# Performance work log

Measured on AMD Instinct MI355X. Metric: run time of the kernel, lower is better.

Reference implementation:

```python
import jax, jax.numpy as jnp
import numpy as np
import math

NEIGHBOR_RADIUS = 30.0

def _masked_softmax(logits, mask, axis):
    # mask: bool, True = keep; all-masked rows return zeros
    p = jax.nn.softmax(jnp.where(mask, logits, -1e9), axis=axis) * mask.astype(logits.dtype)
    return p / jnp.clip(jnp.sum(p, axis=axis, keepdims=True), 1e-9, None)

def _forward(agents_state, agents_mask, map_polylines, map_poly_mask,
             map_poly_type, map_tl_status, map_on_route,
             pm_w1, pm_b1, pm_w2, pm_b2, type_emb, tl_emb, route_emb,
             mo_w1, mo_b1, mo_w2, mo_b2,
             ae_w1, ae_b1, ae_w2, ae_b2, ae_w3, ae_b3,
             mr_w1, mr_b1, mr_w2, mr_b2,
             nr_w1, nr_b1, nr_w2, nr_b2,
             to_w1, to_b1, to_w2, to_b2):
    relu = jax.nn.relu
    a_mask = (agents_mask > 0.5).astype(agents_state.dtype)   # (B,N,T)
    a_feat = agents_state[..., :5]
    # ---- map polyline node encoder ----
    h = relu(map_polylines @ pm_w1 + pm_b1)                   # (B,M,L,H)
    h = relu(h @ pm_w2 + pm_b2)
    h = h.max(axis=2)                                         # (B,M,H) max-pool over points
    t_idx = jnp.clip(map_poly_type, 0, type_emb.shape[0] - 1)
    s_idx = jnp.clip(map_tl_status, 0, tl_emb.shape[0] - 1)
    r_idx = jnp.clip(map_on_route, 0, route_emb.shape[0] - 1)
    h = h + type_emb[t_idx] + tl_emb[s_idx] + route_emb[r_idx]
    h = relu(h @ mo_w1 + mo_b1) @ mo_w2 + mo_b2
    map_mask = map_poly_mask > 0.5                            # (B,M) bool
    map_node = h * map_mask[..., None].astype(h.dtype)        # (B,M,D)
    map_center = map_polylines.mean(axis=2)                   # (B,M,2)
    # ---- agent state encoder ----
    a = relu(a_feat @ ae_w1 + ae_b1)
    a = relu(a @ ae_w2 + ae_b2)
    a_emb = (a @ ae_w3 + ae_b3) * a_mask[..., None]           # (B,N,T,D)
    D = a_emb.shape[-1]
    # ---- agent -> map attention ----
    agent_pos = a_feat[..., 0:2]
    rel = map_center[:, None, None, :, :] - agent_pos[:, :, :, None, :]  # (B,N,T,M,2)
    dist = jnp.linalg.norm(rel, axis=-1, keepdims=True)
    rel_feat = jnp.concatenate([rel, dist], axis=-1)          # (B,N,T,M,3)
    rel_score = (relu(rel_feat @ mr_w1 + mr_b1) @ mr_w2 + mr_b2)[..., 0]  # (B,N,T,M)
    dot = jnp.einsum('bntd,bmd->bntm', a_emb, map_node) / math.sqrt(D)
    score_mask = jnp.broadcast_to(map_mask[:, None, None, :], dot.shape)
    attn = _masked_softmax(dot + rel_score, score_mask, axis=-1)
    map_ctx = jnp.einsum('bntm,bmd->bntd', attn, map_node)    # (B,N,T,D)
    # ---- neighbor graph attention ----
    pos = a_feat[..., 0:2]
    vel = a_feat[..., 3:5]
    pos_j = jnp.transpose(pos, (0, 2, 1, 3))                  # (B,T,N,2)
    vel_j = jnp.transpose(vel, (0, 2, 1, 3))
    rel_pos = pos_j[:, None, :, :, :] - pos[:, :, :, None, :] # (B,N,T,N,2) = p_j - p_i
    rel_vel = vel_j[:, None, :, :, :] - vel[:, :, :, None, :]
    dist_ij = jnp.linalg.norm(rel_pos, axis=-1, keepdims=True)
    rel_ij = jnp.concatenate([rel_pos, rel_vel, dist_ij], axis=-1)        # (B,N,T,N,5)
    nbr_score = (relu(rel_ij @ nr_w1 + nr_b1) @ nr_w2 + nr_b2)[..., 0]    # (B,N,T,N)
    am_b = agents_mask > 0.5
    valid_i = am_b[..., None]                                 # (B,N,T,1)
    valid_j = jnp.transpose(am_b, (0, 2, 1))[:, None, :, :]   # (B,1,T,N)
    N = pos.shape[1]
    not_self = ~jnp.eye(N, dtype=bool)[None, :, None, :]      # (1,N,1,N)
    nbr_mask = valid_i & valid_j & (dist_ij[..., 0] <= NEIGHBOR_RADIUS) & not_self
    dot_n = jnp.einsum('bitd,bjtd->bitj', a_emb, a_emb) / math.sqrt(D)
    w_n = _masked_softmax(dot_n + nbr_score, nbr_mask, axis=-1)
    nbr_ctx = jnp.einsum('bitj,bjtd->bitd', w_n, a_emb)       # (B,N,T,D)
    # ---- tau head ----
    tau = jnp.concatenate([a_emb, map_ctx, nbr_ctx], axis=-1)
    tau = relu(tau @ to_w1 + to_b1) @ to_w2 + to_b2
    return tau * a_mask[..., None]

def setup_inputs() -> dict:
    key = jax.random.key(0)
    B, N, T, M, L = 2, 32, 32, 256, 20
    H, D, TAU = 128, 128, 64
    ks = jax.random.split(key, 32)
    def f(i, shp):
        return jax.random.normal(ks[i], shp, jnp.float32) * 0.05
    inp = {}
    inp['agents_state'] = jax.random.normal(ks[0], (B, N, T, 5), jnp.float32) * jnp.array([50., 50., 1., 5., 5.], jnp.float32)
    inp['agents_mask'] = jnp.ones((B, N, T), jnp.float32)
    inp['map_polylines'] = jax.random.normal(ks[1], (B, M, L, 2), jnp.float32) * 50.0
    inp['map_poly_mask'] = jnp.ones((B, M), jnp.float32)
    inp['map_poly_type'] = jax.random.randint(ks[2], (B, M), 0, 4)
    inp['map_tl_status'] = jax.random.randint(ks[3], (B, M), 0, 8)
    inp['map_on_route'] = jax.random.randint(ks[4], (B, M), 0, 2)
    inp['pm_w1'] = f(5, (2, H));  inp['pm_b1'] = jnp.zeros((H,), jnp.float32)
    inp['pm_w2'] = f(6, (H, H)); inp['pm_b2'] = jnp.zeros((H,), jnp.float32)
    inp['type_emb'] = f(7, (4, H)); inp['tl_emb'] = f(8, (8, H)); inp['route_emb'] = f(9, (2, H))
    inp['mo_w1'] = f(10, (H, H)); inp['mo_b1'] = jnp.zeros((H,), jnp.float32)
    inp['mo_w2'] = f(11, (H, D)); inp['mo_b2'] = jnp.zeros((D,), jnp.float32)
    inp['ae_w1'] = f(12, (5, H)); inp['ae_b1'] = jnp.zeros((H,), jnp.float32)
    inp['ae_w2'] = f(13, (H, H)); inp['ae_b2'] = jnp.zeros((H,), jnp.float32)
    inp['ae_w3'] = f(14, (H, D)); inp['ae_b3'] = jnp.zeros((D,), jnp.float32)
    inp['mr_w1'] = f(15, (3, H)); inp['mr_b1'] = jnp.zeros((H,), jnp.float32)
    inp['mr_w2'] = f(16, (H, 1)); inp['mr_b2'] = jnp.zeros((1,), jnp.float32)
    inp['nr_w1'] = f(17, (5, H)); inp['nr_b1'] = jnp.zeros((H,), jnp.float32)
    inp['nr_w2'] = f(18, (H, 1)); inp['nr_b2'] = jnp.zeros((1,), jnp.float32)
    inp['to_w1'] = f(19, (3 * D, H)); inp['to_b1'] = jnp.zeros((H,), jnp.float32)
    inp['to_w2'] = f(20, (H, TAU)); inp['to_b2'] = jnp.zeros((TAU,), jnp.float32)
    return inp

def reference(agents_state, agents_mask, map_polylines, map_poly_mask,
              map_poly_type, map_tl_status, map_on_route,
              pm_w1, pm_b1, pm_w2, pm_b2, type_emb, tl_emb, route_emb,
              mo_w1, mo_b1, mo_w2, mo_b2,
              ae_w1, ae_b1, ae_w2, ae_b2, ae_w3, ae_b3,
              mr_w1, mr_b1, mr_w2, mr_b2,
              nr_w1, nr_b1, nr_w2, nr_b2,
              to_w1, to_b1, to_w2, to_b2):
    return _forward(agents_state, agents_mask, map_polylines, map_poly_mask,
                    map_poly_type, map_tl_status, map_on_route,
                    pm_w1, pm_b1, pm_w2, pm_b2, type_emb, tl_emb, route_emb,
                    mo_w1, mo_b1, mo_w2, mo_b2,
                    ae_w1, ae_b1, ae_w2, ae_b2, ae_w3, ae_b3,
                    mr_w1, mr_b1, mr_w2, mr_b2,
                    nr_w1, nr_b1, nr_w2, nr_b2,
                    to_w1, to_b1, to_w2, to_b2)
```

## Files before the change

### kernel.cpp

```cpp
#include <hip/hip_runtime.h>

#define RSQRT_D 0.08838834764831843f

__global__ __launch_bounds__(256) void kAB_front(
    const float* __restrict__ poly, const float* __restrict__ pmask,
    const int* __restrict__ ptype, const int* __restrict__ ptl, const int* __restrict__ proute,
    const float* __restrict__ pm_w1, const float* __restrict__ pm_b1,
    const float* __restrict__ pm_w2, const float* __restrict__ pm_b2,
    const float* __restrict__ type_emb, const float* __restrict__ tl_emb, const float* __restrict__ route_emb,
    const float* __restrict__ mo_w1, const float* __restrict__ mo_b1,
    const float* __restrict__ mo_w2, const float* __restrict__ mo_b2,
    const float* __restrict__ astate, const float* __restrict__ amask,
    const float* __restrict__ ae_w1, const float* __restrict__ ae_b1,
    const float* __restrict__ ae_w2, const float* __restrict__ ae_b2,
    const float* __restrict__ ae_w3, const float* __restrict__ ae_b3,
    float* __restrict__ map_node, float* __restrict__ map_nodeT, float* __restrict__ center,
    float* __restrict__ a_emb, float* __restrict__ aT, float* __restrict__ posT)
{
    int tid = threadIdx.x;
    if (blockIdx.x < 512) {
        int bm = blockIdx.x;
        int b = bm >> 8, m = bm & 255;
        int h = tid & 127, rw = tid >> 7;
        __shared__ float xch[2][128];
        __shared__ __align__(16) float hvs[128];
        __shared__ __align__(16) float g2[128];

        const float* pp = poly + bm*40 + rw*20;
        float xs[10], ys[10];
        #pragma unroll
        for (int u = 0; u < 10; ++u) { xs[u] = pp[2*u]; ys[u] = pp[2*u+1]; }
        float acc[10];
        #pragma unroll
        for (int u = 0; u < 10; ++u) acc[u] = 0.f;
        #pragma unroll 4
        for (int k = 0; k < 128; ++k) {
            float w2v = pm_w2[k*128 + h];
            float wx = pm_w1[k], wy = pm_w1[128+k], bb = pm_b1[k];
            #pragma unroll
            for (int u = 0; u < 10; ++u) {
                float h1 = fmaxf(fmaf(wx, xs[u], fmaf(wy, ys[u], bb)), 0.f);
                acc[u] = fmaf(h1, w2v, acc[u]);
            }
        }
        float mx = acc[0];
        #pragma unroll
        for (int u = 1; u < 10; ++u) mx = fmaxf(mx, acc[u]);
        xch[rw][h] = mx;
        __syncthreads();
        if (rw == 0) {
            float v = fmaxf(fmaxf(mx, xch[1][h]) + pm_b2[h], 0.f);
            int ti = min(max(ptype[bm],0),3);
            int si = min(max(ptl[bm],0),7);
            int ri = min(max(proute[bm],0),1);
            hvs[h] = v + type_emb[ti*128+h] + tl_emb[si*128+h] + route_emb[ri*128+h];
        }
        __syncthreads();
        if (rw == 0) {
            float a1 = mo_b1[h];
            for (int kc = 0; kc < 32; ++kc) {
                float4 xv = *(const float4*)&hvs[kc*4];
                a1 = fmaf(xv.x, mo_w1[(kc*4+0)*128+h],
                     fmaf(xv.y, mo_w1[(kc*4+1)*128+h],
                     fmaf(xv.z, mo_w1[(kc*4+2)*128+h],
                     fmaf(xv.w, mo_w1[(kc*4+3)*128+h], a1))));
            }
            g2[h] = fmaxf(a1, 0.f);
        }
        __syncthreads();
        if (rw == 0) {
            float a2 = mo_b2[h];
            for (int kc = 0; kc < 32; ++kc) {
                float4 xv = *(const float4*)&g2[kc*4];
                a2 = fmaf(xv.x, mo_w2[(kc*4+0)*128+h],
                     fmaf(xv.y, mo_w2[(kc*4+1)*128+h],
                     fmaf(xv.z, mo_w2[(kc*4+2)*128+h],
                     fmaf(xv.w, mo_w2[(kc*4+3)*128+h], a2))));
            }
            float mk = (pmask[bm] > 0.5f) ? 1.f : 0.f;
            a2 *= mk;
            map_node[bm*128 + h] = a2;
            map_nodeT[(b*128+h)*256 + m] = a2;
        }
        if (tid == 0) {
            float sx = 0.f, sy = 0.f;
            #pragma unroll
            for (int l = 0; l < 20; ++l) { sx += poly[bm*40 + 2*l]; sy += poly[bm*40 + 2*l + 1]; }
            center[bm*2+0] = sx * 0.05f;
            center[bm*2+1] = sy * 0.05f;
        }
    } else {
        int h = tid & 127, rp = tid >> 7;
        int r0 = (blockIdx.x - 512)*8 + rp*4;
        __shared__ float f5[2][4][5];
        __shared__ __align__(16) float a1s[2][4][128];
        if (h < 20) f5[rp][h/5][h%5] = astate[(r0 + h/5)*5 + (h%5)];
        __syncthreads();
        float b1v = ae_b1[h];
        float v[4];
        {
            float w0 = ae_w1[h], w1 = ae_w1[128+h], w2 = ae_w1[256+h], w3 = ae_w1[384+h], w4 = ae_w1[512+h];
            #pragma unroll
            for (int r = 0; r < 4; ++r) {
                float a = b1v;
                a = fmaf(f5[rp][r][0], w0, a); a = fmaf(f5[rp][r][1], w1, a);
                a = fmaf(f5[rp][r][2], w2, a); a = fmaf(f5[rp][r][3], w3, a);
                a = fmaf(f5[rp][r][4], w4, a);
                v[r] = fmaxf(a, 0.f);
            }
        }
        #pragma unroll
        for (int r = 0; r < 4; ++r) a1s[rp][r][h] = v[r];
        __syncthreads();
        {
            float b2v = ae_b2[h];
            float a0 = b2v, a1 = b2v, a2 = b2v, a3 = b2v;
            for (int kc = 0; kc < 32; ++kc) {
                float4 x0 = *(const float4*)&a1s[rp][0][kc*4];
                float4 x1 = *(const float4*)&a1s[rp][1][kc*4];
                float4 x2 = *(const float4*)&a1s[rp][2][kc*4];
                float4 x3 = *(const float4*)&a1s[rp][3][kc*4];
                float w0 = ae_w2[(kc*4+0)*128+h], w1 = ae_w2[(kc*4+1)*128+h];
                float w2 = ae_w2[(kc*4+2)*128+h], w3 = ae_w2[(kc*4+3)*128+h];
                a0 = fmaf(x0.x,w0,fmaf(x0.y,w1,fmaf(x0.z,w2,fmaf(x0.w,w3,a0))));
                a1 = fmaf(x1.x,w0,fmaf(x1.y,w1,fmaf(x1.z,w2,fmaf(x1.w,w3,a1))));
                a2 = fmaf(x2.x,w0,fmaf(x2.y,w1,fmaf(x2.z,w2,fmaf(x2.w,w3,a2))));
                a3 = fmaf(x3.x,w0,fmaf(x3.y,w1,fmaf(x3.z,w2,fmaf(x3.w,w3,a3))));
            }
            v[0]=fmaxf(a0,0.f); v[1]=fmaxf(a1,0.f); v[2]=fmaxf(a2,0.f); v[3]=fmaxf(a3,0.f);
        }
        __syncthreads();
        #pragma unroll
        for (int r = 0; r < 4; ++r) a1s[rp][r][h] = v[r];
        __syncthreads();
        {
            float b3v = ae_b3[h];
            float a0 = b3v, a1 = b3v, a2 = b3v, a3 = b3v;
            for (int kc = 0; kc < 32; ++kc) {
                float4 x0 = *(const float4*)&a1s[rp][0][kc*4];
                float4 x1 = *(const float4*)&a1s[rp][1][kc*4];
                float4 x2 = *(const float4*)&a1s[rp][2][kc*4];
                float4 x3 = *(const float4*)&a1s[rp][3][kc*4];
                float w0 = ae_w3[(kc*4+0)*128+h], w1 = ae_w3[(kc*4+1)*128+h];
                float w2 = ae_w3[(kc*4+2)*128+h], w3 = ae_w3[(kc*4+3)*128+h];
                a0 = fmaf(x0.x,w0,fmaf(x0.y,w1,fmaf(x0.z,w2,fmaf(x0.w,w3,a0))));
                a1 = fmaf(x1.x,w0,fmaf(x1.y,w1,fmaf(x1.z,w2,fmaf(x1.w,w3,a1))));
                a2 = fmaf(x2.x,w0,fmaf(x2.y,w1,fmaf(x2.z,w2,fmaf(x2.w,w3,a2))));
                a3 = fmaf(x3.x,w0,fmaf(x3.y,w1,fmaf(x3.z,w2,fmaf(x3.w,w3,a3))));
            }
            v[0]=a0; v[1]=a1; v[2]=a2; v[3]=a3;
        }
        #pragma unroll
        for (int r = 0; r < 4; ++r) {
            int rr = r0 + r;
            float mk = (amask[rr] > 0.5f) ? 1.f : 0.f;
            float e = v[r] * mk;
            a_emb[rr*128 + h] = e;
            int bb = rr >> 10, nn = (rr >> 5) & 31, tt = rr & 31;
            int bt = bb*32 + tt;
            aT[(bt*128 + h)*32 + nn] = e;
        }
        if (h < 20) {
            int r = h / 5, c = h % 5;
            int rr = r0 + r;
            int bb = rr >> 10, nn = (rr >> 5) & 31, tt = rr & 31;
            int bt = bb*32 + tt;
            float val;
            if      (c == 0) val = f5[rp][r][0];
            else if (c == 1) val = f5[rp][r][1];
            else if (c == 2) val = f5[rp][r][3];
            else if (c == 3) val = f5[rp][r][4];
            else             val = amask[rr];
            posT[(bt*5 + c)*32 + nn] = val;
        }
    }
}

__global__ __launch_bounds__(256) void kC_attn(
    const float* __restrict__ astate, const float* __restrict__ amask,
    const float* __restrict__ pmask,
    const float* __restrict__ a_emb, const float* __restrict__ map_node,
    const float* __restrict__ map_nodeT, const float* __restrict__ center,
    const float* __restrict__ mr_w1, const float* __restrict__ mr_b1,
    const float* __restrict__ mr_w2, const float* __restrict__ mr_b2,
    const float* __restrict__ aT, const float* __restrict__ posT,
    const float* __restrict__ nr_w1, const float* __restrict__ nr_b1,
    const float* __restrict__ nr_w2, const float* __restrict__ nr_b2,
    float* __restrict__ map_ctx, float* __restrict__ p_n)
{
    int tid = threadIdx.x;
    int lam = tid & 63, wv = tid >> 6;
    __shared__ float lg4[4][256];
    __shared__ __align__(16) float p4[256*4];
    __shared__ float ctxp[4][128];

    if (blockIdx.x < 512) {
        int r0 = blockIdx.x * 4;
        int b = r0 >> 10;
        int m = tid;
        float rx[4], ry[4], dd[4], dt[4], sA[4];
        float b2c = mr_b2[0];
        float cx = center[(b*256+m)*2+0], cy = center[(b*256+m)*2+1];
        #pragma unroll
        for (int r = 0; r < 4; ++r) {
            float px = astate[(r0+r)*5+0], py = astate[(r0+r)*5+1];
            rx[r] = cx - px; ry[r] = cy - py;
            dd[r] = sqrtf(rx[r]*rx[r] + ry[r]*ry[r]);
            dt[r] = 0.f; sA[r] = b2c;
        }
        #pragma unroll 8
        for (int hh = 0; hh < 128; ++hh) {
            float wa = mr_w1[hh], wb = mr_w1[128+hh], wc = mr_w1[256+hh];
            float bb = mr_b1[hh], w2 = mr_w2[hh];
            #pragma unroll
            for (int r = 0; r < 4; ++r) {
                float t1 = fmaf(rx[r], wa, fmaf(ry[r], wb, fmaf(dd[r], wc, bb)));
                sA[r] = fmaf(fmaxf(t1, 0.f), w2, sA[r]);
            }
        }
        const float* mT = map_nodeT + b*128*256 + m;
        #pragma unroll 8
        for (int d = 0; d < 128; ++d) {
            float v = mT[d*256];
            #pragma unroll
            for (int r = 0; r < 4; ++r)
                dt[r] = fmaf(v, a_emb[(r0+r)*128 + d], dt[r]);
        }
        bool mk = pmask[b*256+m] > 0.5f;
        #pragma unroll
        for (int r = 0; r < 4; ++r)
            lg4[r][m] = mk ? fmaf(dt[r], RSQRT_D, sA[r]) : -1e30f;
        __syncthreads();
        {
            float x0 = lg4[wv][lam], x1 = lg4[wv][64+lam], x2 = lg4[wv][128+lam], x3 = lg4[wv][192+lam];
            float mxv = fmaxf(fmaxf(x0,x1), fmaxf(x2,x3));
            #pragma unroll
            for (int off = 32; off; off >>= 1) mxv = fmaxf(mxv, __shfl_xor(mxv, off));
            float e0 = (x0 > -1e29f) ? expf(x0-mxv) : 0.f;
            float e1 = (x1 > -1e29f) ? expf(x1-mxv) : 0.f;
            float e2 = (x2 > -1e29f) ? expf(x2-mxv) : 0.f;
            float e3 = (x3 > -1e29f) ? expf(x3-mxv) : 0.f;
            float sm = e0+e1+e2+e3;
            #pragma unroll
            for (int off = 32; off; off >>= 1) sm += __shfl_xor(sm, off);
            float inv = 1.f / fmaxf(sm, 1e-9f);
            p4[lam*4 + wv]       = e0*inv;
            p4[(64+lam)*4 + wv]  = e1*inv;
            p4[(128+lam)*4 + wv] = e2*inv;
            p4[(192+lam)*4 + wv] = e3*inv;
        }
        __syncthreads();
        {
            int d = tid & 127, hf = tid >> 7;
            float ac0 = 0.f, ac1 = 0.f, ac2 = 0.f, ac3 = 0.f;
            const float* mn = map_node + (b*256 + hf*128)*128 + d;
            const float4* pp = (const float4*)p4 + hf*128;
            #pragma unroll 4
            for (int mm = 0; mm < 128; ++mm) {
                float4 pv = pp[mm];
                float v = mn[mm*128];
                ac0 = fmaf(pv.x, v, ac0); ac1 = fmaf(pv.y, v, ac1);
                ac2 = fmaf(pv.z, v, ac2); ac3 = fmaf(pv.w, v, ac3);
            }
            if (hf == 1) { ctxp[0][d]=ac0; ctxp[1][d]=ac1; ctxp[2][d]=ac2; ctxp[3][d]=ac3; }
            __syncthreads();
            if (hf == 0) {
                map_ctx[(r0+0)*128+d] = ac0 + ctxp[0][d];
                map_ctx[(r0+1)*128+d] = ac1 + ctxp[1][d];
                map_ctx[(r0+2)*128+d] = ac2 + ctxp[2][d];
                map_ctx[(r0+3)*128+d] = ac3 + ctxp[3][d];
            }
        }
    } else {
        int r = (blockIdx.x - 512)*4 + wv;
        int b = r >> 10, ii = (r >> 5) & 31, tt = r & 31;
        int bt = b*32 + tt;
        int j = lam & 31, hs = lam >> 5;
        float pxi = astate[r*5+0], pyi = astate[r*5+1], vxi = astate[r*5+3], vyi = astate[r*5+4];
        const float* pT = posT + bt*160;
        float pxj = pT[j], pyj = pT[32+j], vxj = pT[64+j], vyj = pT[96+j], mj = pT[128+j];
        float rpx = pxj-pxi, rpy = pyj-pyi, rvx = vxj-vxi, rvy = vyj-vyi;
        float ddv = sqrtf(rpx*rpx + rpy*rpy);
        const float* ei = a_emb + (size_t)r*128;
        const float* aTp = aT + (size_t)bt*4096 + j;
        float s = 0.f, dot = 0.f;
        int h0 = hs*64;
        #pragma unroll 8
        for (int q = 0; q < 64; ++q) {
            int hh = h0 + q;
            float wA = nr_w1[hh], wB = nr_w1[128+hh], wC = nr_w1[256+hh];
            float wD = nr_w1[384+hh], wE = nr_w1[512+hh];
            float bb = nr_b1[hh], w2 = nr_w2[hh];
            float t1 = fmaf(rpx, wA, fmaf(rpy, wB, fmaf(rvx, wC,
                       fmaf(rvy, wD, fmaf(ddv, wE, bb)))));
            s = fmaf(fmaxf(t1, 0.f), w2, s);
            dot = fmaf(ei[hh], aTp[hh*32], dot);
        }
        s   += __shfl_xor(s, 32);
        dot += __shfl_xor(dot, 32);
        bool vi = amask[r] > 0.5f, vj = mj > 0.5f;
        bool ok = vi && vj && (ddv <= 30.0f) && (j != ii);
        float lg = ok ? fmaf(dot, RSQRT_D, s + nr_b2[0]) : -1e30f;
        float mxv = lg;
        #pragma unroll
        for (int off = 16; off; off >>= 1) mxv = fmaxf(mxv, __shfl_xor(mxv, off));
        float e = (lg > -1e29f) ? expf(lg - mxv) : 0.f;
        float sm = e;
        #pragma unroll
        for (int off = 16; off; off >>= 1) sm += __shfl_xor(sm, off);
        if (hs == 0) p_n[r*32 + j] = e / fmaxf(sm, 1e-9f);
    }
}

__global__ __launch_bounds__(256) void kD_out(
    const float* __restrict__ amask, const float* __restrict__ a_emb,
    const float* __restrict__ map_ctx, const float* __restrict__ p_n,
    const float* __restrict__ to_w1, const float* __restrict__ to_b1,
    const float* __restrict__ to_w2, const float* __restrict__ to_b2,
    float* __restrict__ out)
{
    int r0 = blockIdx.x * 4;
    int b = r0 >> 10, t0 = r0 & 31;
    int tid = threadIdx.x;
    __shared__ __align__(16) float tau[4][384];
    __shared__ float redn[4][128];
    __shared__ __align__(16) float gpart[4][4][128];
    __shared__ __align__(16) float g1s[4][128];

    for (int q = tid; q < 512; q += 256) {
        int rr = q >> 7, d = q & 127;
        tau[rr][d]       = a_emb[(r0+rr)*128 + d];
        tau[rr][128 + d] = map_ctx[(r0+rr)*128 + d];
    }
    __syncthreads();
    {
        int d = tid & 127, hf = tid >> 7;
        float ac[4] = {0.f,0.f,0.f,0.f};
        for (int jj = 0; jj < 16; ++jj) {
            int j2 = hf*16 + jj;
            float p0 = p_n[(r0+0)*32 + j2];
            float p1 = p_n[(r0+1)*32 + j2];
            float p2 = p_n[(r0+2)*32 + j2];
            float p3 = p_n[(r0+3)*32 + j2];
            const float* ejb = a_emb + (size_t)((b*32 + j2)*32 + t0)*128 + d;
            ac[0] = fmaf(p0, ejb[0],   ac[0]);
            ac[1] = fmaf(p1, ejb[128], ac[1]);
            ac[2] = fmaf(p2, ejb[256], ac[2]);
            ac[3] = fmaf(p3, ejb[384], ac[3]);
        }
        if (hf == 1) { redn[0][d]=ac[0]; redn[1][d]=ac[1]; redn[2][d]=ac[2]; redn[3][d]=ac[3]; }
        __syncthreads();
        if (hf == 0) {
            #pragma unroll
            for (int r = 0; r < 4; ++r) tau[r][256 + d] = ac[r] + redn[r][d];
        }
    }
    __syncthreads();
    {
        int h6 = tid & 63, kq = tid >> 6;
        float aL[4] = {0.f,0.f,0.f,0.f};
        float aH[4] = {0.f,0.f,0.f,0.f};
        for (int c = 0; c < 24; ++c) {
            int k4 = kq*24 + c;
            float4 x0 = *(const float4*)&tau[0][k4*4];
            float4 x1 = *(const float4*)&tau[1][k4*4];
            float4 x2 = *(const float4*)&tau[2][k4*4];
            float4 x3 = *(const float4*)&tau[3][k4*4];
            float wl0 = to_w1[(k4*4+0)*128 + h6], wh0 = to_w1[(k4*4+0)*128 + 64+h6];
            float wl1 = to_w1[(k4*4+1)*128 + h6], wh1 = to_w1[(k4*4+1)*128 + 64+h6];
            float wl2 = to_w1[(k4*4+2)*128 + h6], wh2 = to_w1[(k4*4+2)*128 + 64+h6];
            float wl3 = to_w1[(k4*4+3)*128 + h6], wh3 = to_w1[(k4*4+3)*128 + 64+h6];
            aL[0]=fmaf(x0.x,wl0,fmaf(x0.y,wl1,fmaf(x0.z,wl2,fmaf(x0.w,wl3,aL[0]))));
            aH[0]=fmaf(x0.x,wh0,fmaf(x0.y,wh1,fmaf(x0.z,wh2,fmaf(x0.w,wh3,aH[0]))));
            aL[1]=fmaf(x1.x,wl0,fmaf(x1.y,wl1,fmaf(x1.z,wl2,fmaf(x1.w,wl3,aL[1]))));
            aH[1]=fmaf(x1.x,wh0,fmaf(x1.y,wh1,fmaf(x1.z,wh2,fmaf(x1.w,wh3,aH[1]))));
            aL[2]=fmaf(x2.x,wl0,fmaf(x2.y,wl1,fmaf(x2.z,wl2,fmaf(x2.w,wl3,aL[2]))));
            aH[2]=fmaf(x2.x,wh0,fmaf(x2.y,wh1,fmaf(x2.z,wh2,fmaf(x2.w,wh3,aH[2]))));
            aL[3]=fmaf(x3.x,wl0,fmaf(x3.y,wl1,fmaf(x3.z,wl2,fmaf(x3.w,wl3,aL[3]))));
            aH[3]=fmaf(x3.x,wh0,fmaf(x3.y,wh1,fmaf(x3.z,wh2,fmaf(x3.w,wh3,aH[3]))));
        }
        #pragma unroll
        for (int r = 0; r < 4; ++r) {
            gpart[kq][r][h6]      = aL[r];
            gpart[kq][r][64 + h6] = aH[r];
        }
    }
    __syncthreads();
    {
        int h = tid & 127, rp = tid >> 7;
        float bv = to_b1[h];
        #pragma unroll
        for (int rr = rp; rr < 4; rr += 2) {
            float s = gpart[0][rr][h] + gpart[1][rr][h] + gpart[2][rr][h] + gpart[3][rr][h];
            g1s[rr][h] = fmaxf(s + bv, 0.f);
        }
    }
    __syncthreads();
    {
        int o = tid & 63, row = tid >> 6;
        float a2 = to_b2[o];
        for (int kc = 0; kc < 32; ++kc) {
            float4 g = *(const float4*)&g1s[row][kc*4];
            a2 = fmaf(g.x, to_w2[(kc*4+0)*64 + o],
                 fmaf(g.y, to_w2[(kc*4+1)*64 + o],
                 fmaf(g.z, to_w2[(kc*4+2)*64 + o],
                 fmaf(g.w, to_w2[(kc*4+3)*64 + o], a2))));
        }
        float mk = (amask[r0+row] > 0.5f) ? 1.f : 0.f;
        out[(r0+row)*64 + o] = a2 * mk;
    }
}

extern "C" void kernel_launch(void* const* d_in, const int* in_sizes, int n_in,
                              void* d_out, int out_size, void* d_ws, size_t ws_size,
                              hipStream_t stream) {
    const float* agents_state  = (const float*)d_in[0];
    const float* agents_mask   = (const float*)d_in[1];
    const float* map_polylines = (const float*)d_in[2];
    const float* map_poly_mask = (const float*)d_in[3];
    const int*   map_poly_type = (const int*)d_in[4];
    const int*   map_tl_status = (const int*)d_in[5];
    const int*   map_on_route  = (const int*)d_in[6];
    const float* pm_w1 = (const float*)d_in[7];
    const float* pm_b1 = (const float*)d_in[8];
    const float* pm_w2 = (const float*)d_in[9];
    const float* pm_b2 = (const float*)d_in[10];
    const float* type_emb  = (const float*)d_in[11];
    const float* tl_emb    = (const float*)d_in[12];
    const float* route_emb = (const float*)d_in[13];
    const float* mo_w1 = (const float*)d_in[14];
    const float* mo_b1 = (const float*)d_in[15];
    const float* mo_w2 = (const float*)d_in[16];
    const float* mo_b2 = (const float*)d_in[17];
    const float* ae_w1 = (const float*)d_in[18];
    const float* ae_b1 = (const float*)d_in[19];
    const float* ae_w2 = (const float*)d_in[20];
    const float* ae_b2 = (const float*)d_in[21];
    const float* ae_w3 = (const float*)d_in[22];
    const float* ae_b3 = (const float*)d_in[23];
    const float* mr_w1 = (const float*)d_in[24];
    const float* mr_b1 = (const float*)d_in[25];
    const float* mr_w2 = (const float*)d_in[26];
    const float* mr_b2 = (const float*)d_in[27];
    const float* nr_w1 = (const float*)d_in[28];
    const float* nr_b1 = (const float*)d_in[29];
    const float* nr_w2 = (const float*)d_in[30];
    const float* nr_b2 = (const float*)d_in[31];
    const float* to_w1 = (const float*)d_in[32];
    const float* to_b1 = (const float*)d_in[33];
    const float* to_w2 = (const float*)d_in[34];
    const float* to_b2 = (const float*)d_in[35];

    float* ws = (float*)d_ws;
    float* map_node  = ws;
    float* map_nodeT = ws + 65536;
    float* center    = ws + 131072;
    float* a_emb     = ws + 132096;
    float* aT        = ws + 394240;
    float* posT      = ws + 656384;
    float* map_ctx   = ws + 666624;
    float* p_n       = ws + 928768;

    float* out = (float*)d_out;

    kAB_front<<<768, 256, 0, stream>>>(map_polylines, map_poly_mask,
        map_poly_type, map_tl_status, map_on_route,
        pm_w1, pm_b1, pm_w2, pm_b2, type_emb, tl_emb, route_emb,
        mo_w1, mo_b1, mo_w2, mo_b2,
        agents_state, agents_mask,
        ae_w1, ae_b1, ae_w2, ae_b2, ae_w3, ae_b3,
        map_node, map_nodeT, center, a_emb, aT, posT);

    kC_attn<<<1024, 256, 0, stream>>>(agents_state, agents_mask, map_poly_mask,
        a_emb, map_node, map_nodeT, center,
        mr_w1, mr_b1, mr_w2, mr_b2,
        aT, posT,
        nr_w1, nr_b1, nr_w2, nr_b2,
        map_ctx, p_n);

    kD_out<<<512, 256, 0, stream>>>(agents_mask, a_emb, map_ctx, p_n,
        to_w1, to_b1, to_w2, to_b2, out);
}
```

Baseline: 188.9 us.

## Fuse attention and output kernels; stage polyline hidden layer in shared memory

The map-attention, neighbor-attention and output-MLP kernels are merged into one 512-thread kernel per 4-row group. The map and neighbor halves run in parallel thread groups, and context vectors and neighbor probabilities pass through shared memory instead of global buffers. This removes one launch and the map_ctx/p_n round trip to global memory. Separately, the polyline encoder now computes the first-layer activations once per hidden unit into shared memory rather than recomputing them inside the k loop. The cost is larger blocks and more shared memory, which can lower occupancy, and half the threads sit idle in the later stages.

```diff
diff --git a/kernel.cpp b/kernel.cpp
--- a/kernel.cpp
+++ b/kernel.cpp
@@ -25,23 +25,48 @@
         __shared__ float xch[2][128];
         __shared__ __align__(16) float hvs[128];
         __shared__ __align__(16) float g2[128];
-
-        const float* pp = poly + bm*40 + rw*20;
-        float xs[10], ys[10];
-        #pragma unroll
-        for (int u = 0; u < 10; ++u) { xs[u] = pp[2*u]; ys[u] = pp[2*u+1]; }
-        float acc[10];
-        #pragma unroll
-        for (int u = 0; u < 10; ++u) acc[u] = 0.f;
-        #pragma unroll 4
-        for (int k = 0; k < 128; ++k) {
-            float w2v = pm_w2[k*128 + h];
+        __shared__ __align__(16) float h1s[2][128][12];
+
+        {
+            int k = h;
+            int half = rw;
+            const float* pp = poly + bm*40 + half*20;
             float wx = pm_w1[k], wy = pm_w1[128+k], bb = pm_b1[k];
+            float h1v[10];
             #pragma unroll
             for (int u = 0; u < 10; ++u) {
-                float h1 = fmaxf(fmaf(wx, xs[u], fmaf(wy, ys[u], bb)), 0.f);
-                acc[u] = fmaf(h1, w2v, acc[u]);
-            }
+                float x = pp[2*u], y = pp[2*u+1];
+                h1v[u] = fmaxf(fmaf(wx, x, fmaf(wy, y, bb)), 0.f);
+            }
+            float4 s0 = make_float4(h1v[0], h1v[1], h1v[2], h1v[3]);
+            float4 s1 = make_float4(h1v[4], h1v[5], h1v[6], h1v[7]);
+            float2 s2 = make_float2(h1v[8], h1v[9]);
+            *(float4*)&h1s[half][k][0] = s0;
+            *(float4*)&h1s[half][k][4] = s1;
+            *(float2*)&h1s[half][k][8] = s2;
+        }
+        __syncthreads();
+
+        float acc[10];
+        #pragma unroll
+        for (int u = 0; u < 10; ++u) acc[u] = 0.f;
+        const float* w2p = pm_w2 + h;
+        #pragma unroll 2
+        for (int k = 0; k < 128; ++k) {
+            float w2v = w2p[k*128];
+            float4 A  = *(const float4*)&h1s[rw][k][0];
+            float4 Bv = *(const float4*)&h1s[rw][k][4];
+            float2 Cv = *(const float2*)&h1s[rw][k][8];
+            acc[0] = fmaf(A.x,  w2v, acc[0]);
+            acc[1] = fmaf(A.y,  w2v, acc[1]);
+            acc[2] = fmaf(A.z,  w2v, acc[2]);
+            acc[3] = fmaf(A.w,  w2v, acc[3]);
+            acc[4] = fmaf(Bv.x, w2v, acc[4]);
+            acc[5] = fmaf(Bv.y, w2v, acc[5]);
+            acc[6] = fmaf(Bv.z, w2v, acc[6]);
+            acc[7] = fmaf(Bv.w, w2v, acc[7]);
+            acc[8] = fmaf(Cv.x, w2v, acc[8]);
+            acc[9] = fmaf(Cv.y, w2v, acc[9]);
         }
         float mx = acc[0];
         #pragma unroll
@@ -176,7 +201,7 @@
     }
 }
 
-__global__ __launch_bounds__(256) void kC_attn(
+__global__ __launch_bounds__(512) void kCD_fused(
     const float* __restrict__ astate, const float* __restrict__ amask,
     const float* __restrict__ pmask,
     const float* __restrict__ a_emb, const float* __restrict__ map_node,
@@ -186,17 +211,24 @@
     const float* __restrict__ aT, const float* __restrict__ posT,
     const float* __restrict__ nr_w1, const float* __restrict__ nr_b1,
     const float* __restrict__ nr_w2, const float* __restrict__ nr_b2,
-    float* __restrict__ map_ctx, float* __restrict__ p_n)
+    const float* __restrict__ to_w1, const float* __restrict__ to_b1,
+    const float* __restrict__ to_w2, const float* __restrict__ to_b2,
+    float* __restrict__ out)
 {
     int tid = threadIdx.x;
-    int lam = tid & 63, wv = tid >> 6;
+    int r0 = blockIdx.x * 4;
+    int b = r0 >> 10, t0 = r0 & 31;
+
     __shared__ float lg4[4][256];
     __shared__ __align__(16) float p4[256*4];
     __shared__ float ctxp[4][128];
-
-    if (blockIdx.x < 512) {
-        int r0 = blockIdx.x * 4;
-        int b = r0 >> 10;
+    __shared__ float pj[4][32];
+    __shared__ __align__(16) float tau[4][384];
+    __shared__ float redn[4][128];
+    __shared__ __align__(16) float gpart[4][4][128];
+    __shared__ __align__(16) float g1s[4][128];
+
+    if (tid < 256) {
         int m = tid;
         float rx[4], ry[4], dd[4], dt[4], sA[4];
         float b2c = mr_b2[0];
@@ -230,50 +262,10 @@
         #pragma unroll
         for (int r = 0; r < 4; ++r)
             lg4[r][m] = mk ? fmaf(dt[r], RSQRT_D, sA[r]) : -1e30f;
-        __syncthreads();
-        {
-            float x0 = lg4[wv][lam], x1 = lg4[wv][64+lam], x2 = lg4[wv][128+lam], x3 = lg4[wv][192+lam];
-            float mxv = fmaxf(fmaxf(x0,x1), fmaxf(x2,x3));
-            #pragma unroll
-            for (int off = 32; off; off >>= 1) mxv = fmaxf(mxv, __shfl_xor(mxv, off));
-            float e0 = (x0 > -1e29f) ? expf(x0-mxv) : 0.f;
-            float e1 = (x1 > -1e29f) ? expf(x1-mxv) : 0.f;
-            float e2 = (x2 > -1e29f) ? expf(x2-mxv) : 0.f;
-            float e3 = (x3 > -1e29f) ? expf(x3-mxv) : 0.f;
-            float sm = e0+e1+e2+e3;
-            #pragma unroll
-            for (int off = 32; off; off >>= 1) sm += __shfl_xor(sm, off);
-            float inv = 1.f / fmaxf(sm, 1e-9f);
-            p4[lam*4 + wv]       = e0*inv;
-            p4[(64+lam)*4 + wv]  = e1*inv;
-            p4[(128+lam)*4 + wv] = e2*inv;
-            p4[(192+lam)*4 + wv] = e3*inv;
-        }
-        __syncthreads();
-        {
-            int d = tid & 127, hf = tid >> 7;
-            float ac0 = 0.f, ac1 = 0.f, ac2 = 0.f, ac3 = 0.f;
-            const float* mn = map_node + (b*256 + hf*128)*128 + d;
-            const float4* pp = (const float4*)p4 + hf*128;
-            #pragma unroll 4
-            for (int mm = 0; mm < 128; ++mm) {
-                float4 pv = pp[mm];
-                float v = mn[mm*128];
-                ac0 = fmaf(pv.x, v, ac0); ac1 = fmaf(pv.y, v, ac1);
-                ac2 = fmaf(pv.z, v, ac2); ac3 = fmaf(pv.w, v, ac3);
-            }
-            if (hf == 1) { ctxp[0][d]=ac0; ctxp[1][d]=ac1; ctxp[2][d]=ac2; ctxp[3][d]=ac3; }
-            __syncthreads();
-            if (hf == 0) {
-                map_ctx[(r0+0)*128+d] = ac0 + ctxp[0][d];
-                map_ctx[(r0+1)*128+d] = ac1 + ctxp[1][d];
-                map_ctx[(r0+2)*128+d] = ac2 + ctxp[2][d];
-                map_ctx[(r0+3)*128+d] = ac3 + ctxp[3][d];
-            }
-        }
     } else {
-        int r = (blockIdx.x - 512)*4 + wv;
-        int b = r >> 10, ii = (r >> 5) & 31, tt = r & 31;
+        int lam = tid & 63, wv = (tid >> 6) & 3;
+        int r = r0 + wv;
+        int ii = (r >> 5) & 31, tt = r & 31;
         int bt = b*32 + tt;
         int j = lam & 31, hs = lam >> 5;
         float pxi = astate[r*5+0], pyi = astate[r*5+1], vxi = astate[r*5+3], vyi = astate[r*5+4];
@@ -308,55 +300,85 @@
         float sm = e;
         #pragma unroll
         for (int off = 16; off; off >>= 1) sm += __shfl_xor(sm, off);
-        if (hs == 0) p_n[r*32 + j] = e / fmaxf(sm, 1e-9f);
-    }
-}
-
-__global__ __launch_bounds__(256) void kD_out(
-    const float* __restrict__ amask, const float* __restrict__ a_emb,
-    const float* __restrict__ map_ctx, const float* __restrict__ p_n,
-    const float* __restrict__ to_w1, const float* __restrict__ to_b1,
-    const float* __restrict__ to_w2, const float* __restrict__ to_b2,
-    float* __restrict__ out)
-{
-    int r0 = blockIdx.x * 4;
-    int b = r0 >> 10, t0 = r0 & 31;
-    int tid = threadIdx.x;
-    __shared__ __align__(16) float tau[4][384];
-    __shared__ float redn[4][128];
-    __shared__ __align__(16) float gpart[4][4][128];
-    __shared__ __align__(16) float g1s[4][128];
-
-    for (int q = tid; q < 512; q += 256) {
-        int rr = q >> 7, d = q & 127;
-        tau[rr][d]       = a_emb[(r0+rr)*128 + d];
-        tau[rr][128 + d] = map_ctx[(r0+rr)*128 + d];
-    }
-    __syncthreads();
-    {
+        if (hs == 0) pj[wv][j] = e / fmaxf(sm, 1e-9f);
+    }
+    __syncthreads();
+
+    if (tid < 256) {
+        int lam = tid & 63, wv = tid >> 6;
+        float x0 = lg4[wv][lam], x1 = lg4[wv][64+lam], x2 = lg4[wv][128+lam], x3 = lg4[wv][192+lam];
+        float mxv = fmaxf(fmaxf(x0,x1), fmaxf(x2,x3));
+        #pragma unroll
+        for (int off = 32; off; off >>= 1) mxv = fmaxf(mxv, __shfl_xor(mxv, off));
+        float e0 = (x0 > -1e29f) ? expf(x0-mxv) : 0.f;
+        float e1 = (x1 > -1e29f) ? expf(x1-mxv) : 0.f;
+        float e2 = (x2 > -1e29f) ? expf(x2-mxv) : 0.f;
+        float e3 = (x3 > -1e29f) ? expf(x3-mxv) : 0.f;
+        float sm = e0+e1+e2+e3;
+        #pragma unroll
+        for (int off = 32; off; off >>= 1) sm += __shfl_xor(sm, off);
+        float inv = 1.f / fmaxf(sm, 1e-9f);
+        p4[lam*4 + wv]       = e0*inv;
+        p4[(64+lam)*4 + wv]  = e1*inv;
+        p4[(128+lam)*4 + wv] = e2*inv;
+        p4[(192+lam)*4 + wv] = e3*inv;
+    } else {
+        int idx = tid - 256;
+        int d = idx & 127, rr = idx >> 7;
+        tau[rr][d]   = a_emb[(r0+rr)*128 + d];
+        tau[rr+2][d] = a_emb[(r0+rr+2)*128 + d];
+    }
+    __syncthreads();
+
+    float pv0 = 0.f, pv1 = 0.f, pv2 = 0.f, pv3 = 0.f;
+    if (tid < 256) {
         int d = tid & 127, hf = tid >> 7;
-        float ac[4] = {0.f,0.f,0.f,0.f};
+        const float* mn = map_node + (b*256 + hf*128)*128 + d;
+        const float4* ppv = (const float4*)p4 + hf*128;
+        #pragma unroll 4
+        for (int mm = 0; mm < 128; ++mm) {
+            float4 pvv = ppv[mm];
+            float v = mn[mm*128];
+            pv0 = fmaf(pvv.x, v, pv0); pv1 = fmaf(pvv.y, v, pv1);
+            pv2 = fmaf(pvv.z, v, pv2); pv3 = fmaf(pvv.w, v, pv3);
+        }
+        if (hf == 1) { ctxp[0][d]=pv0; ctxp[1][d]=pv1; ctxp[2][d]=pv2; ctxp[3][d]=pv3; }
+    }
+    __syncthreads();
+    if (tid < 128) {
+        int d = tid;
+        tau[0][128+d] = pv0 + ctxp[0][d];
+        tau[1][128+d] = pv1 + ctxp[1][d];
+        tau[2][128+d] = pv2 + ctxp[2][d];
+        tau[3][128+d] = pv3 + ctxp[3][d];
+    }
+    __syncthreads();
+
+    float na0 = 0.f, na1 = 0.f, na2 = 0.f, na3 = 0.f;
+    if (tid < 256) {
+        int d = tid & 127, hf = tid >> 7;
         for (int jj = 0; jj < 16; ++jj) {
             int j2 = hf*16 + jj;
-            float p0 = p_n[(r0+0)*32 + j2];
-            float p1 = p_n[(r0+1)*32 + j2];
-            float p2 = p_n[(r0+2)*32 + j2];
-            float p3 = p_n[(r0+3)*32 + j2];
+            float p0 = pj[0][j2], p1 = pj[1][j2], p2 = pj[2][j2], p3 = pj[3][j2];
             const float* ejb = a_emb + (size_t)((b*32 + j2)*32 + t0)*128 + d;
-            ac[0] = fmaf(p0, ejb[0],   ac[0]);
-            ac[1] = fmaf(p1, ejb[128], ac[1]);
-            ac[2] = fmaf(p2, ejb[256], ac[2]);
-            ac[3] = fmaf(p3, ejb[384], ac[3]);
-        }
-        if (hf == 1) { redn[0][d]=ac[0]; redn[1][d]=ac[1]; redn[2][d]=ac[2]; redn[3][d]=ac[3]; }
-        __syncthreads();
-        if (hf == 0) {
-            #pragma unroll
-            for (int r = 0; r < 4; ++r) tau[r][256 + d] = ac[r] + redn[r][d];
-        }
-    }
-    __syncthreads();
-    {
+            na0 = fmaf(p0, ejb[0],   na0);
+            na1 = fmaf(p1, ejb[128], na1);
+            na2 = fmaf(p2, ejb[256], na2);
+            na3 = fmaf(p3, ejb[384], na3);
+        }
+        if (hf == 1) { redn[0][d]=na0; redn[1][d]=na1; redn[2][d]=na2; redn[3][d]=na3; }
+    }
+    __syncthreads();
+    if (tid < 128) {
+        int d = tid;
+        tau[0][256+d] = na0 + redn[0][d];
+        tau[1][256+d] = na1 + redn[1][d];
+        tau[2][256+d] = na2 + redn[2][d];
+        tau[3][256+d] = na3 + redn[3][d];
+    }
+    __syncthreads();
+
+    if (tid < 256) {
         int h6 = tid & 63, kq = tid >> 6;
         float aL[4] = {0.f,0.f,0.f,0.f};
         float aH[4] = {0.f,0.f,0.f,0.f};
@@ -386,7 +408,7 @@
         }
     }
     __syncthreads();
-    {
+    if (tid < 256) {
         int h = tid & 127, rp = tid >> 7;
         float bv = to_b1[h];
         #pragma unroll
@@ -396,7 +418,7 @@
         }
     }
     __syncthreads();
-    {
+    if (tid < 256) {
         int o = tid & 63, row = tid >> 6;
         float a2 = to_b2[o];
         for (int kc = 0; kc < 32; ++kc) {
@@ -458,8 +480,6 @@
     float* a_emb     = ws + 132096;
     float* aT        = ws + 394240;
     float* posT      = ws + 656384;
-    float* map_ctx   = ws + 666624;
-    float* p_n       = ws + 928768;
 
     float* out = (float*)d_out;
 
@@ -471,13 +491,11 @@
         ae_w1, ae_b1, ae_w2, ae_b2, ae_w3, ae_b3,
         map_node, map_nodeT, center, a_emb, aT, posT);
 
-    kC_attn<<<1024, 256, 0, stream>>>(agents_state, agents_mask, map_poly_mask,
+    kCD_fused<<<512, 512, 0, stream>>>(agents_state, agents_mask, map_poly_mask,
         a_emb, map_node, map_nodeT, center,
         mr_w1, mr_b1, mr_w2, mr_b2,
         aT, posT,
         nr_w1, nr_b1, nr_w2, nr_b2,
-        map_ctx, p_n);
-
-    kD_out<<<512, 256, 0, stream>>>(agents_mask, a_emb, map_ctx, p_n,
-        to_w1, to_b1, to_w2, to_b2, out);
+        to_w1, to_b1, to_w2, to_b2,
+        out);
 }
```

Measured after the change: 195.9 us. 1.04x slower.
